# Performance work log

Measured on AMD Instinct MI355X. Metric: run time of the kernel, lower is better.

Reference implementation:

```python
import jax, jax.numpy as jnp
import numpy as np

K = 1024  # attention hidden dim
H = 1024  # encoder hidden dim


def setup_inputs() -> dict:
    key = jax.random.key(0)
    ks = jax.random.split(key, 8)
    B, S = 32, 2048
    decoder_state = jax.random.normal(ks[0], (B, H), dtype=jnp.float32)
    encoder_hiddens = jax.random.normal(ks[1], (B, S, H), dtype=jnp.float32)
    # Linear params (torch convention: y = x @ W.T + b)
    Wa_w = jax.random.normal(ks[2], (1, K), dtype=jnp.float32) / np.sqrt(K)
    Wa_b = jnp.zeros((1,), dtype=jnp.float32)
    Wb_w = jax.random.normal(ks[3], (K, H), dtype=jnp.float32) / np.sqrt(H)
    Wb_b = jnp.zeros((K,), dtype=jnp.float32)
    Wc_w = jax.random.normal(ks[4], (K, H), dtype=jnp.float32) / np.sqrt(H)
    Wc_b = jnp.zeros((K,), dtype=jnp.float32)
    return {
        "decoder_state": decoder_state,
        "encoder_hiddens": encoder_hiddens,
        "Wa_w": Wa_w, "Wa_b": Wa_b,
        "Wb_w": Wb_w, "Wb_b": Wb_b,
        "Wc_w": Wc_w, "Wc_b": Wc_b,
    }


def reference(decoder_state, encoder_hiddens, Wa_w, Wa_b, Wb_w, Wb_b, Wc_w, Wc_b):
    # dec_proj: [B, K]; enc_proj: [B, S, K]
    dec_proj = decoder_state @ Wb_w.T + Wb_b
    enc_proj = jnp.einsum('bsh,kh->bsk', encoder_hiddens, Wc_w) + Wc_b
    # additive score: tanh then project to scalar -> [B, S]
    e = jnp.tanh(dec_proj[:, None, :] + enc_proj)
    scores = jnp.einsum('bsk,k->bs', e, Wa_w[0]) + Wa_b[0]
    attn = jax.nn.softmax(scores, axis=1)
    # weighted sum over sequence -> [B, H]
    context = jnp.einsum('bs,bsh->bh', attn, encoder_hiddens)
    return context
```

## Files before the change

kernel.cpp:

```cpp
#include <hip/hip_runtime.h>
#include <hip/hip_bf16.h>
#include <stdint.h>

#define B_SZ 32
#define S_SZ 2048
#define H_SZ 1024
#define K_SZ 1024
#define M_SZ (B_SZ * S_SZ)

typedef __attribute__((ext_vector_type(8))) short bf16x8;
typedef __attribute__((ext_vector_type(4))) float f32x4;


__device__ __forceinline__ short f2bf_rne(float f) {
    uint32_t u = __builtin_bit_cast(uint32_t, f);
    u += 0x7fffu + ((u >> 16) & 1u);
    return (short)(u >> 16);
}

__device__ __forceinline__ float bf2f(unsigned short u) {
    return __builtin_bit_cast(float, (uint32_t)u << 16);
}

__device__ __forceinline__ float fast_tanh(float x) {
    float ex = __expf(2.0f * x);
    return 1.0f - 2.0f / (ex + 1.0f);
}


__global__ void cvt_bf16_k(const float* __restrict__ in,
                           __hip_bfloat16* __restrict__ out, int n8) {
    int idx = blockIdx.x * blockDim.x + threadIdx.x;
    int stride = gridDim.x * blockDim.x;
    for (int i = idx; i < n8; i += stride) {
        const float4* p = (const float4*)in + (size_t)i * 2;
        float4 a = p[0], b = p[1];
        bf16x8 r;
        r[0] = f2bf_rne(a.x); r[1] = f2bf_rne(a.y);
        r[2] = f2bf_rne(a.z); r[3] = f2bf_rne(a.w);
        r[4] = f2bf_rne(b.x); r[5] = f2bf_rne(b.y);
        r[6] = f2bf_rne(b.z); r[7] = f2bf_rne(b.w);
        ((bf16x8*)out)[i] = r;
    }
}


__global__ __launch_bounds__(256) void decproj_k(
    const float* __restrict__ ds, const float* __restrict__ Wb,
    const float* __restrict__ Wb_b, const float* __restrict__ Wc_b,
    float* __restrict__ dp) {
    int g = blockIdx.x * 4 + (threadIdx.x >> 6);
    int lane = threadIdx.x & 63;
    int b = g >> 10;
    int k = g & 1023;
    const float4* wrow = (const float4*)(Wb + (size_t)k * H_SZ);
    const float4* xrow = (const float4*)(ds + (size_t)b * H_SZ);
    float sum = 0.f;
#pragma unroll
    for (int it = 0; it < 4; it++) {
        float4 w = wrow[lane + it * 64];
        float4 x = xrow[lane + it * 64];
        sum += w.x * x.x + w.y * x.y + w.z * x.z + w.w * x.w;
    }
#pragma unroll
    for (int off = 1; off < 64; off <<= 1) sum += __shfl_xor(sum, off, 64);
    if (lane == 0) dp[g] = sum + Wb_b[k] + Wc_b[k];
}


template <bool AF32>
__global__ __launch_bounds__(256) void gemm_scores_k(
    const void* __restrict__ Aptr, const __hip_bfloat16* __restrict__ Bw,
    const float* __restrict__ decp, const float* __restrict__ Wa,
    float* __restrict__ sp) {
    constexpr int ABYTES = AF32 ? 128 * 32 * 4 : 128 * 32 * 2;
    __shared__ __align__(16) unsigned char AsmRaw[ABYTES];
    __shared__ __align__(16) unsigned char BsmRaw[128 * 32 * 2];

    const int t = threadIdx.x;
    const int wave = t >> 6;
    const int lane = t & 63;
    const int wm = wave >> 1, wn = wave & 1;
    const int quad = lane >> 4;
    const int l15 = lane & 15;

    const int id = blockIdx.x;
    const int colBlk = (id >> 3) & 7;
    const int rowBlk = ((id >> 6) << 3) | (id & 7);
    const int row0 = rowBlk * 128;
    const int col0 = colBlk * 128;
    const int b = row0 >> 11;

    f32x4 acc[4][4];
#pragma unroll
    for (int i = 0; i < 4; i++)
#pragma unroll
        for (int j = 0; j < 4; j++) acc[i][j] = f32x4{0.f, 0.f, 0.f, 0.f};

    const __hip_bfloat16* Ab = (const __hip_bfloat16*)Aptr;
    const float* Af = (const float*)Aptr;

    for (int k0 = 0; k0 < H_SZ; k0 += 32) {
        if constexpr (AF32) {
#pragma unroll
            for (int inst = 0; inst < 4; inst++) {
                int slot = inst * 256 + t;
                int r = slot >> 3, c4 = slot & 7;
                const float* g = Af + (size_t)(row0 + r) * H_SZ + k0 + c4 * 4;
                __builtin_amdgcn_global_load_lds(
                    (const __attribute__((address_space(1))) void*)g,
                    (__attribute__((address_space(3))) void*)(AsmRaw + inst * 4096 + wave * 1024),
                    16, 0, 0);
            }
        } else {
#pragma unroll
            for (int inst = 0; inst < 2; inst++) {
                int slot = inst * 256 + t;
                int r = slot >> 2, c8 = slot & 3;
                const __hip_bfloat16* g = Ab + (size_t)(row0 + r) * H_SZ + k0 + c8 * 8;
                __builtin_amdgcn_global_load_lds(
                    (const __attribute__((address_space(1))) void*)g,
                    (__attribute__((address_space(3))) void*)(AsmRaw + inst * 4096 + wave * 1024),
                    16, 0, 0);
            }
        }
#pragma unroll
        for (int inst = 0; inst < 2; inst++) {
            int slot = inst * 256 + t;
            int r = slot >> 2, c8 = slot & 3;
            const __hip_bfloat16* g = Bw + (size_t)(col0 + r) * H_SZ + k0 + c8 * 8;
            __builtin_amdgcn_global_load_lds(
                (const __attribute__((address_space(1))) void*)g,
                (__attribute__((address_space(3))) void*)(BsmRaw + inst * 4096 + wave * 1024),
                16, 0, 0);
        }
        __syncthreads();

        bf16x8 afr[4], bfr[4];
#pragma unroll
        for (int i = 0; i < 4; i++) {
            int r = wm * 64 + i * 16 + l15;
            if constexpr (AF32) {
                const float* ap = (const float*)AsmRaw + r * 32 + quad * 8;
                f32x4 lo = *(const f32x4*)ap;
                f32x4 hi = *(const f32x4*)(ap + 4);
                bf16x8 v;
                v[0] = f2bf_rne(lo[0]); v[1] = f2bf_rne(lo[1]);
                v[2] = f2bf_rne(lo[2]); v[3] = f2bf_rne(lo[3]);
                v[4] = f2bf_rne(hi[0]); v[5] = f2bf_rne(hi[1]);
                v[6] = f2bf_rne(hi[2]); v[7] = f2bf_rne(hi[3]);
                afr[i] = v;
            } else {
                afr[i] = *(const bf16x8*)((const __hip_bfloat16*)AsmRaw + r * 32 + quad * 8);
            }
        }
#pragma unroll
        for (int j = 0; j < 4; j++) {
            int r = wn * 64 + j * 16 + l15;
            bfr[j] = *(const bf16x8*)((const __hip_bfloat16*)BsmRaw + r * 32 + quad * 8);
        }
#pragma unroll
        for (int i = 0; i < 4; i++)
#pragma unroll
            for (int j = 0; j < 4; j++)
                acc[i][j] = __builtin_amdgcn_mfma_f32_16x16x32_bf16(afr[i], bfr[j], acc[i][j], 0, 0, 0);
        __syncthreads();
    }

    float wa_j[4], dp_j[4];
#pragma unroll
    for (int j = 0; j < 4; j++) {
        int c = col0 + wn * 64 + j * 16 + l15;
        wa_j[j] = Wa[c];
        dp_j[j] = decp[b * K_SZ + c];
    }
    const int slotIdx = colBlk * 2 + wn;
#pragma unroll
    for (int i = 0; i < 4; i++) {
#pragma unroll
        for (int r = 0; r < 4; r++) {
            float tsum = 0.f;
#pragma unroll
            for (int j = 0; j < 4; j++)
                tsum += wa_j[j] * fast_tanh(acc[i][j][r] + dp_j[j]);
#pragma unroll
            for (int off = 1; off < 16; off <<= 1) tsum += __shfl_xor(tsum, off, 64);
            if (l15 == 0) {
                int m = row0 + wm * 64 + i * 16 + quad * 4 + r;
                sp[(size_t)slotIdx * M_SZ + m] = tsum;
            }
        }
    }
}


__global__ __launch_bounds__(256) void softmax_k(
    const float* __restrict__ sp, float* __restrict__ attn) {
    int b = blockIdx.x;
    int t = threadIdx.x;
    __shared__ float wred[4];
    __shared__ float wred2[4];
    float sc[8];
    float mx = -1e30f;
#pragma unroll
    for (int u = 0; u < 8; u++) {
        int m = b * S_SZ + t + u * 256;
        float v = 0.f;
#pragma unroll
        for (int c = 0; c < 16; c++) v += sp[(size_t)c * M_SZ + m];
        sc[u] = v;
        mx = fmaxf(mx, v);
    }
#pragma unroll
    for (int off = 1; off < 64; off <<= 1) mx = fmaxf(mx, __shfl_xor(mx, off, 64));
    if ((t & 63) == 0) wred[t >> 6] = mx;
    __syncthreads();
    mx = fmaxf(fmaxf(wred[0], wred[1]), fmaxf(wred[2], wred[3]));
    float lsum = 0.f;
#pragma unroll
    for (int u = 0; u < 8; u++) { sc[u] = expf(sc[u] - mx); lsum += sc[u]; }
#pragma unroll
    for (int off = 1; off < 64; off <<= 1) lsum += __shfl_xor(lsum, off, 64);
    if ((t & 63) == 0) wred2[t >> 6] = lsum;
    __syncthreads();
    float inv = 1.f / (wred2[0] + wred2[1] + wred2[2] + wred2[3]);
#pragma unroll
    for (int u = 0; u < 8; u++) attn[b * S_SZ + t + u * 256] = sc[u] * inv;
}


template <bool BF16E>
__global__ __launch_bounds__(256) void ctx_part_k(
    const float* __restrict__ attn, const void* __restrict__ encp,
    float* __restrict__ cp) {
    int b = blockIdx.x >> 5;
    int c = blockIdx.x & 31;
    int t = threadIdx.x;
    __shared__ float wloc[64];
    if (t < 64) wloc[t] = attn[b * S_SZ + c * 64 + t];
    __syncthreads();
    float4 acc = {0.f, 0.f, 0.f, 0.f};
    if constexpr (BF16E) {
        const ushort4* ep = (const ushort4*)((const __hip_bfloat16*)encp +
                              ((size_t)b * S_SZ + (size_t)c * 64) * H_SZ);
#pragma unroll 8
        for (int s = 0; s < 64; s++) {
            float w = wloc[s];
            ushort4 v = ep[s * 256 + t];
            acc.x += w * bf2f(v.x); acc.y += w * bf2f(v.y);
            acc.z += w * bf2f(v.z); acc.w += w * bf2f(v.w);
        }
    } else {
        const float4* ep = (const float4*)((const float*)encp +
                              ((size_t)b * S_SZ + (size_t)c * 64) * H_SZ);
#pragma unroll 8
        for (int s = 0; s < 64; s++) {
            float w = wloc[s];
            float4 v = ep[s * 256 + t];
            acc.x += w * v.x; acc.y += w * v.y;
            acc.z += w * v.z; acc.w += w * v.w;
        }
    }
    ((float4*)(cp + ((size_t)c * B_SZ + b) * H_SZ))[t] = acc;
}

__global__ void ctx_red_k(const float* __restrict__ cp, float* __restrict__ out) {
    int i = blockIdx.x * blockDim.x + threadIdx.x;
    float s = 0.f;
#pragma unroll
    for (int c = 0; c < 32; c++) s += cp[(size_t)c * (B_SZ * H_SZ) + i];
    out[i] = s;
}


extern "C" void kernel_launch(void* const* d_in, const int* in_sizes, int n_in,
                              void* d_out, int out_size, void* d_ws, size_t ws_size,
                              hipStream_t stream) {
    const float* dec  = (const float*)d_in[0];
    const float* enc  = (const float*)d_in[1];
    const float* Wa_w = (const float*)d_in[2];
    const float* Wb_w = (const float*)d_in[4];
    const float* Wb_b = (const float*)d_in[5];
    const float* Wc_w = (const float*)d_in[6];
    const float* Wc_b = (const float*)d_in[7];
    float* out = (float*)d_out;

    char* ws = (char*)d_ws;
    size_t off = 0;
    auto alloc = [&](size_t bytes) -> void* {
        void* p = ws + off;
        off += (bytes + 255) & ~(size_t)255;
        return p;
    };
    __hip_bfloat16* wc_bf = (__hip_bfloat16*)alloc((size_t)K_SZ * H_SZ * 2);
    float* dp     = (float*)alloc((size_t)B_SZ * K_SZ * 4);
    float* spart  = (float*)alloc((size_t)16 * M_SZ * 4);
    float* attn   = (float*)alloc((size_t)B_SZ * S_SZ * 4);
    float* cpart  = (float*)alloc((size_t)32 * B_SZ * H_SZ * 4);
    __hip_bfloat16* enc_bf = (__hip_bfloat16*)alloc((size_t)M_SZ * H_SZ * 2);
    const bool useBf16A = (off <= ws_size);

    cvt_bf16_k<<<512, 256, 0, stream>>>(Wc_w, wc_bf, K_SZ * H_SZ / 8);
    if (useBf16A)
        cvt_bf16_k<<<8192, 256, 0, stream>>>(enc, enc_bf, M_SZ * H_SZ / 8);
    decproj_k<<<8192, 256, 0, stream>>>(dec, Wb_w, Wb_b, Wc_b, dp);
    if (useBf16A)
        gemm_scores_k<false><<<(M_SZ / 128) * 8, 256, 0, stream>>>(enc_bf, wc_bf, dp, Wa_w, spart);
    else
        gemm_scores_k<true><<<(M_SZ / 128) * 8, 256, 0, stream>>>(enc, wc_bf, dp, Wa_w, spart);
    softmax_k<<<B_SZ, 256, 0, stream>>>(spart, attn);
    if (useBf16A)
        ctx_part_k<true><<<B_SZ * 32, 256, 0, stream>>>(attn, enc_bf, cpart);
    else
        ctx_part_k<false><<<B_SZ * 32, 256, 0, stream>>>(attn, enc, cpart);
    ctx_red_k<<<128, 256, 0, stream>>>(cpart, out);
}
```

Measured before the change: 613.5 us.

## Switch score GEMM to 32x32x16 MFMA with K=64 stage, fuse prep kernels

The bf16 score GEMM now uses 32x32x16 MFMA tiles with a 64-wide K step per barrier pair, halving the number of synchronisations and cutting LDS fragment reads per MFMA. The epilogue is remapped to the 32x32 accumulator layout. The Wc conversion and decoder projection are merged into one launch, and softmax uses 1024 threads per batch row. These changes aim to reduce GEMM sync and LDS overhead plus launch count, at the cost of more LDS per block and possible bank conflicts in the unpadded layout.

```diff
diff --git a/kernel.cpp b/kernel.cpp
--- a/kernel.cpp
+++ b/kernel.cpp
@@ -10,6 +10,7 @@
 
 typedef __attribute__((ext_vector_type(8))) short bf16x8;
 typedef __attribute__((ext_vector_type(4))) float f32x4;
+typedef __attribute__((ext_vector_type(16))) float f32x16;
 
 
 __device__ __forceinline__ short f2bf_rne(float f) {
@@ -45,11 +46,24 @@
 }
 
 
-__global__ __launch_bounds__(256) void decproj_k(
+__global__ __launch_bounds__(256) void prep_k(
+    const float* __restrict__ Wc, __hip_bfloat16* __restrict__ wc_bf,
     const float* __restrict__ ds, const float* __restrict__ Wb,
     const float* __restrict__ Wb_b, const float* __restrict__ Wc_b,
     float* __restrict__ dp) {
-    int g = blockIdx.x * 4 + (threadIdx.x >> 6);
+    if (blockIdx.x < 512) {
+        int i = blockIdx.x * 256 + threadIdx.x;
+        const float4* p = (const float4*)Wc + (size_t)i * 2;
+        float4 a = p[0], b = p[1];
+        bf16x8 r;
+        r[0] = f2bf_rne(a.x); r[1] = f2bf_rne(a.y);
+        r[2] = f2bf_rne(a.z); r[3] = f2bf_rne(a.w);
+        r[4] = f2bf_rne(b.x); r[5] = f2bf_rne(b.y);
+        r[6] = f2bf_rne(b.z); r[7] = f2bf_rne(b.w);
+        ((bf16x8*)wc_bf)[i] = r;
+        return;
+    }
+    int g = (blockIdx.x - 512) * 4 + (threadIdx.x >> 6);
     int lane = threadIdx.x & 63;
     int b = g >> 10;
     int k = g & 1023;
@@ -68,61 +82,129 @@
 }
 
 
-template <bool AF32>
-__global__ __launch_bounds__(256) void gemm_scores_k(
-    const void* __restrict__ Aptr, const __hip_bfloat16* __restrict__ Bw,
+__global__ __launch_bounds__(256) void gemm_scores32_k(
+    const __hip_bfloat16* __restrict__ Ab, const __hip_bfloat16* __restrict__ Bw,
     const float* __restrict__ decp, const float* __restrict__ Wa,
     float* __restrict__ sp) {
-    constexpr int ABYTES = AF32 ? 128 * 32 * 4 : 128 * 32 * 2;
-    __shared__ __align__(16) unsigned char AsmRaw[ABYTES];
+    __shared__ __align__(16) unsigned char AsmRaw[2 * 128 * 32 * 2];
+    __shared__ __align__(16) unsigned char BsmRaw[2 * 128 * 32 * 2];
+
+    const int t = threadIdx.x;
+    const int wave = t >> 6;
+    const int lane = t & 63;
+    const int wm = wave >> 1, wn = wave & 1;
+    const int l31 = lane & 31;
+    const int half = lane >> 5;
+
+    const int id = blockIdx.x;
+    const int colBlk = (id >> 3) & 7;
+    const int rowBlk = ((id >> 6) << 3) | (id & 7);
+    const int row0 = rowBlk * 128;
+    const int col0 = colBlk * 128;
+    const int b = row0 >> 11;
+
+    f32x16 acc[2][2];
+#pragma unroll
+    for (int i = 0; i < 2; i++)
+#pragma unroll
+        for (int j = 0; j < 2; j++)
+#pragma unroll
+            for (int r = 0; r < 16; r++) acc[i][j][r] = 0.f;
+
+    for (int k0 = 0; k0 < H_SZ; k0 += 64) {
+#pragma unroll
+        for (int p = 0; p < 2; p++)
+#pragma unroll
+            for (int inst = 0; inst < 2; inst++) {
+                int slot = inst * 256 + t;
+                int r = slot >> 2, c8 = slot & 3;
+                const __hip_bfloat16* gA = Ab + (size_t)(row0 + r) * H_SZ + k0 + p * 32 + c8 * 8;
+                __builtin_amdgcn_global_load_lds(
+                    (const __attribute__((address_space(1))) void*)gA,
+                    (__attribute__((address_space(3))) void*)(AsmRaw + p * 8192 + inst * 4096 + wave * 1024),
+                    16, 0, 0);
+                const __hip_bfloat16* gB = Bw + (size_t)(col0 + r) * H_SZ + k0 + p * 32 + c8 * 8;
+                __builtin_amdgcn_global_load_lds(
+                    (const __attribute__((address_space(1))) void*)gB,
+                    (__attribute__((address_space(3))) void*)(BsmRaw + p * 8192 + inst * 4096 + wave * 1024),
+                    16, 0, 0);
+            }
+        __syncthreads();
+
+#pragma unroll
+        for (int ks = 0; ks < 4; ks++) {
+            const int pOff = (ks >> 1) * 8192;
+            const int cOff = (ks & 1) * 32 + half * 16;
+            bf16x8 a0 = *(const bf16x8*)(AsmRaw + pOff + (wm * 64 + l31) * 64 + cOff);
+            bf16x8 a1 = *(const bf16x8*)(AsmRaw + pOff + (wm * 64 + 32 + l31) * 64 + cOff);
+            bf16x8 b0 = *(const bf16x8*)(BsmRaw + pOff + (wn * 64 + l31) * 64 + cOff);
+            bf16x8 b1 = *(const bf16x8*)(BsmRaw + pOff + (wn * 64 + 32 + l31) * 64 + cOff);
+            acc[0][0] = __builtin_amdgcn_mfma_f32_32x32x16_bf16(a0, b0, acc[0][0], 0, 0, 0);
+            acc[0][1] = __builtin_amdgcn_mfma_f32_32x32x16_bf16(a0, b1, acc[0][1], 0, 0, 0);
+            acc[1][0] = __builtin_amdgcn_mfma_f32_32x32x16_bf16(a1, b0, acc[1][0], 0, 0, 0);
+            acc[1][1] = __builtin_amdgcn_mfma_f32_32x32x16_bf16(a1, b1, acc[1][1], 0, 0, 0);
+        }
+        __syncthreads();
+    }
+
+    float wa_j[2], dp_j[2];
+#pragma unroll
+    for (int j = 0; j < 2; j++) {
+        int c = col0 + wn * 64 + j * 32 + l31;
+        wa_j[j] = Wa[c];
+        dp_j[j] = decp[b * K_SZ + c];
+    }
+    const int slotIdx = colBlk * 2 + wn;
+#pragma unroll
+    for (int i = 0; i < 2; i++) {
+#pragma unroll
+        for (int r = 0; r < 16; r++) {
+            float v = wa_j[0] * fast_tanh(acc[i][0][r] + dp_j[0])
+                    + wa_j[1] * fast_tanh(acc[i][1][r] + dp_j[1]);
+#pragma unroll
+            for (int off = 1; off < 32; off <<= 1) v += __shfl_xor(v, off, 64);
+            if (l31 == 0) {
+                int m = row0 + wm * 64 + i * 32 + (r & 3) + 8 * (r >> 2) + 4 * half;
+                sp[(size_t)slotIdx * M_SZ + m] = v;
+            }
+        }
+    }
+}
+
+
+__global__ __launch_bounds__(256) void gemm_scores_f32_k(
+    const float* __restrict__ Af, const __hip_bfloat16* __restrict__ Bw,
+    const float* __restrict__ decp, const float* __restrict__ Wa,
+    float* __restrict__ sp) {
+    __shared__ __align__(16) unsigned char AsmRaw[128 * 32 * 4];
     __shared__ __align__(16) unsigned char BsmRaw[128 * 32 * 2];
-
     const int t = threadIdx.x;
     const int wave = t >> 6;
     const int lane = t & 63;
     const int wm = wave >> 1, wn = wave & 1;
     const int quad = lane >> 4;
     const int l15 = lane & 15;
-
     const int id = blockIdx.x;
     const int colBlk = (id >> 3) & 7;
     const int rowBlk = ((id >> 6) << 3) | (id & 7);
     const int row0 = rowBlk * 128;
     const int col0 = colBlk * 128;
     const int b = row0 >> 11;
-
     f32x4 acc[4][4];
 #pragma unroll
     for (int i = 0; i < 4; i++)
 #pragma unroll
         for (int j = 0; j < 4; j++) acc[i][j] = f32x4{0.f, 0.f, 0.f, 0.f};
-
-    const __hip_bfloat16* Ab = (const __hip_bfloat16*)Aptr;
-    const float* Af = (const float*)Aptr;
-
     for (int k0 = 0; k0 < H_SZ; k0 += 32) {
-        if constexpr (AF32) {
-#pragma unroll
-            for (int inst = 0; inst < 4; inst++) {
-                int slot = inst * 256 + t;
-                int r = slot >> 3, c4 = slot & 7;
-                const float* g = Af + (size_t)(row0 + r) * H_SZ + k0 + c4 * 4;
-                __builtin_amdgcn_global_load_lds(
-                    (const __attribute__((address_space(1))) void*)g,
-                    (__attribute__((address_space(3))) void*)(AsmRaw + inst * 4096 + wave * 1024),
-                    16, 0, 0);
-            }
-        } else {
-#pragma unroll
-            for (int inst = 0; inst < 2; inst++) {
-                int slot = inst * 256 + t;
-                int r = slot >> 2, c8 = slot & 3;
-                const __hip_bfloat16* g = Ab + (size_t)(row0 + r) * H_SZ + k0 + c8 * 8;
-                __builtin_amdgcn_global_load_lds(
-                    (const __attribute__((address_space(1))) void*)g,
-                    (__attribute__((address_space(3))) void*)(AsmRaw + inst * 4096 + wave * 1024),
-                    16, 0, 0);
-            }
+#pragma unroll
+        for (int inst = 0; inst < 4; inst++) {
+            int slot = inst * 256 + t;
+            int r = slot >> 3, c4 = slot & 7;
+            const float* g = Af + (size_t)(row0 + r) * H_SZ + k0 + c4 * 4;
+            __builtin_amdgcn_global_load_lds(
+                (const __attribute__((address_space(1))) void*)g,
+                (__attribute__((address_space(3))) void*)(AsmRaw + inst * 4096 + wave * 1024),
+                16, 0, 0);
         }
 #pragma unroll
         for (int inst = 0; inst < 2; inst++) {
@@ -135,24 +217,19 @@
                 16, 0, 0);
         }
         __syncthreads();
-
         bf16x8 afr[4], bfr[4];
 #pragma unroll
         for (int i = 0; i < 4; i++) {
             int r = wm * 64 + i * 16 + l15;
-            if constexpr (AF32) {
-                const float* ap = (const float*)AsmRaw + r * 32 + quad * 8;
-                f32x4 lo = *(const f32x4*)ap;
-                f32x4 hi = *(const f32x4*)(ap + 4);
-                bf16x8 v;
-                v[0] = f2bf_rne(lo[0]); v[1] = f2bf_rne(lo[1]);
-                v[2] = f2bf_rne(lo[2]); v[3] = f2bf_rne(lo[3]);
-                v[4] = f2bf_rne(hi[0]); v[5] = f2bf_rne(hi[1]);
-                v[6] = f2bf_rne(hi[2]); v[7] = f2bf_rne(hi[3]);
-                afr[i] = v;
-            } else {
-                afr[i] = *(const bf16x8*)((const __hip_bfloat16*)AsmRaw + r * 32 + quad * 8);
-            }
+            const float* ap = (const float*)AsmRaw + r * 32 + quad * 8;
+            f32x4 lo = *(const f32x4*)ap;
+            f32x4 hi = *(const f32x4*)(ap + 4);
+            bf16x8 v;
+            v[0] = f2bf_rne(lo[0]); v[1] = f2bf_rne(lo[1]);
+            v[2] = f2bf_rne(lo[2]); v[3] = f2bf_rne(lo[3]);
+            v[4] = f2bf_rne(hi[0]); v[5] = f2bf_rne(hi[1]);
+            v[6] = f2bf_rne(hi[2]); v[7] = f2bf_rne(hi[3]);
+            afr[i] = v;
         }
 #pragma unroll
         for (int j = 0; j < 4; j++) {
@@ -166,7 +243,6 @@
                 acc[i][j] = __builtin_amdgcn_mfma_f32_16x16x32_bf16(afr[i], bfr[j], acc[i][j], 0, 0, 0);
         __syncthreads();
     }
-
     float wa_j[4], dp_j[4];
 #pragma unroll
     for (int j = 0; j < 4; j++) {
@@ -194,17 +270,17 @@
 }
 
 
-__global__ __launch_bounds__(256) void softmax_k(
+__global__ __launch_bounds__(1024) void softmax_k(
     const float* __restrict__ sp, float* __restrict__ attn) {
     int b = blockIdx.x;
     int t = threadIdx.x;
-    __shared__ float wred[4];
-    __shared__ float wred2[4];
-    float sc[8];
+    __shared__ float wred[16];
+    __shared__ float wred2[16];
+    float sc[2];
     float mx = -1e30f;
 #pragma unroll
-    for (int u = 0; u < 8; u++) {
-        int m = b * S_SZ + t + u * 256;
+    for (int u = 0; u < 2; u++) {
+        int m = b * S_SZ + t + u * 1024;
         float v = 0.f;
 #pragma unroll
         for (int c = 0; c < 16; c++) v += sp[(size_t)c * M_SZ + m];
@@ -215,17 +291,21 @@
     for (int off = 1; off < 64; off <<= 1) mx = fmaxf(mx, __shfl_xor(mx, off, 64));
     if ((t & 63) == 0) wred[t >> 6] = mx;
     __syncthreads();
-    mx = fmaxf(fmaxf(wred[0], wred[1]), fmaxf(wred[2], wred[3]));
+#pragma unroll
+    for (int w = 0; w < 16; w++) mx = fmaxf(mx, wred[w]);
     float lsum = 0.f;
 #pragma unroll
-    for (int u = 0; u < 8; u++) { sc[u] = expf(sc[u] - mx); lsum += sc[u]; }
+    for (int u = 0; u < 2; u++) { sc[u] = expf(sc[u] - mx); lsum += sc[u]; }
 #pragma unroll
     for (int off = 1; off < 64; off <<= 1) lsum += __shfl_xor(lsum, off, 64);
     if ((t & 63) == 0) wred2[t >> 6] = lsum;
     __syncthreads();
-    float inv = 1.f / (wred2[0] + wred2[1] + wred2[2] + wred2[3]);
-#pragma unroll
-    for (int u = 0; u < 8; u++) attn[b * S_SZ + t + u * 256] = sc[u] * inv;
+    float tot = 0.f;
+#pragma unroll
+    for (int w = 0; w < 16; w++) tot += wred2[w];
+    float inv = 1.f / tot;
+#pragma unroll
+    for (int u = 0; u < 2; u++) attn[b * S_SZ + t + u * 1024] = sc[u] * inv;
 }
 
 
@@ -300,15 +380,14 @@
     __hip_bfloat16* enc_bf = (__hip_bfloat16*)alloc((size_t)M_SZ * H_SZ * 2);
     const bool useBf16A = (off <= ws_size);
 
-    cvt_bf16_k<<<512, 256, 0, stream>>>(Wc_w, wc_bf, K_SZ * H_SZ / 8);
-    if (useBf16A)
+    prep_k<<<512 + 8192, 256, 0, stream>>>(Wc_w, wc_bf, dec, Wb_w, Wb_b, Wc_b, dp);
+    if (useBf16A) {
         cvt_bf16_k<<<8192, 256, 0, stream>>>(enc, enc_bf, M_SZ * H_SZ / 8);
-    decproj_k<<<8192, 256, 0, stream>>>(dec, Wb_w, Wb_b, Wc_b, dp);
-    if (useBf16A)
-        gemm_scores_k<false><<<(M_SZ / 128) * 8, 256, 0, stream>>>(enc_bf, wc_bf, dp, Wa_w, spart);
-    else
-        gemm_scores_k<true><<<(M_SZ / 128) * 8, 256, 0, stream>>>(enc, wc_bf, dp, Wa_w, spart);
-    softmax_k<<<B_SZ, 256, 0, stream>>>(spart, attn);
+        gemm_scores32_k<<<(M_SZ / 128) * 8, 256, 0, stream>>>(enc_bf, wc_bf, dp, Wa_w, spart);
+    } else {
+        gemm_scores_f32_k<<<(M_SZ / 128) * 8, 256, 0, stream>>>(enc, wc_bf, dp, Wa_w, spart);
+    }
+    softmax_k<<<B_SZ, 1024, 0, stream>>>(spart, attn);
     if (useBf16A)
         ctx_part_k<true><<<B_SZ * 32, 256, 0, stream>>>(attn, enc_bf, cpart);
     else
```

Result: slower. 649.0 us (+5.8%).
